# Performance work log

Measured on AMD Instinct MI355X. Metric: run time of the kernel, lower is better.

The kernel has to match this reference:

```python
import jax, jax.numpy as jnp
import numpy as np

N, E, IN, H, D, C = 30000, 400000, 128, 4, 64, 40
EPS = 1e-5
SLOPE = 0.2  # DGL GATv2Conv leaky_relu negative_slope default


def setup_inputs() -> dict:
    key = jax.random.key(0)
    ks = jax.random.split(key, 20)
    def rn(k, shape, s=0.05):
        return jax.random.normal(k, shape, jnp.float32) * s
    return {
        "x": jax.random.normal(ks[0], (N, IN), jnp.float32),
        "src": jax.random.randint(ks[1], (E,), 0, N),
        "dst": jax.random.randint(ks[2], (E,), 0, N),
        # layer 0: in=128 -> heads*64 (residual projection since 128 != 256)
        "W_src0": rn(ks[3], (IN, H * D)), "W_dst0": rn(ks[4], (IN, H * D)),
        "b0": jnp.zeros((H * D,), jnp.float32), "attn0": rn(ks[5], (H, D)),
        "res_W0": rn(ks[6], (IN, H * D)),
        # layer 1: 256 -> heads*64 (identity residual since 256 == 256)
        "W_src1": rn(ks[7], (H * D, H * D)), "W_dst1": rn(ks[8], (H * D, H * D)),
        "b1": jnp.zeros((H * D,), jnp.float32), "attn1": rn(ks[9], (H, D)),
        # layer 2: 256 -> heads*40 (residual projection)
        "W_src2": rn(ks[10], (H * D, H * C)), "W_dst2": rn(ks[11], (H * D, H * C)),
        "b2": jnp.zeros((H * C,), jnp.float32), "attn2": rn(ks[12], (H, C)),
        "res_W2": rn(ks[13], (H * D, H * C)),
        # batchnorm affine params (training-mode batch stats)
        "g0": jnp.ones((H * D,), jnp.float32), "be0": jnp.zeros((H * D,), jnp.float32),
        "g1": jnp.ones((H * D,), jnp.float32), "be1": jnp.zeros((H * D,), jnp.float32),
    }


def gatv2_layer(h, src, dst, Wsrc, Wdst, b, attn, resW, out_dim, relu_act):
    # DGL GATv2Conv: score_e = attn . leaky_relu(fc_src(h)[u] + fc_dst(h)[v])
    n = h.shape[0]
    fs = (h @ Wsrc).reshape(n, H, out_dim)
    fd = (h @ Wdst).reshape(n, H, out_dim)
    e = jax.nn.leaky_relu(fs[src] + fd[dst], SLOPE)      # [E, H, out]
    score = jnp.einsum("ehd,hd->eh", e, attn)            # [E, H]
    # segment softmax over incoming edges of each dst node
    m = jax.ops.segment_max(score, dst, num_segments=n)
    m = jnp.where(jnp.isfinite(m), m, 0.0)               # zero in-degree safety
    ex = jnp.exp(score - m[dst])
    denom = jax.ops.segment_sum(ex, dst, num_segments=n)
    alpha = ex / jnp.maximum(denom, 1e-9)[dst]
    rst = jax.ops.segment_sum(alpha[:, :, None] * fs[src], dst, num_segments=n)
    res = (h @ resW).reshape(n, H, out_dim) if resW is not None else h.reshape(n, H, out_dim)
    rst = rst + res + b.reshape(1, H, out_dim)
    return jax.nn.relu(rst) if relu_act else rst


def batchnorm(h, g, be):
    mu = h.mean(0)
    var = h.var(0)  # biased variance, as torch BN uses for normalization
    return g * (h - mu) * jax.lax.rsqrt(var + EPS) + be


def reference(x, src, dst, W_src0, W_dst0, b0, attn0, res_W0, W_src1, W_dst1, b1, attn1, W_src2, W_dst2, b2, attn2, res_W2, g0, be0, g1, be1):
    h = gatv2_layer(x, src, dst, W_src0, W_dst0, b0, attn0, res_W0, D, True)
    h = jax.nn.relu(batchnorm(h.reshape(N, H * D), g0, be0))  # dropout = identity (eval)
    h = gatv2_layer(h, src, dst, W_src1, W_dst1, b1, attn1, None, D, True)
    h = jax.nn.relu(batchnorm(h.reshape(N, H * D), g1, be1))
    h = gatv2_layer(h, src, dst, W_src2, W_dst2, b2, attn2, res_W2, C, False)
    h = h.mean(1)  # mean over heads -> [N, C]
    return jax.nn.log_softmax(h, axis=-1)
```

## Files before the change

kernel.cpp:

```cpp
#include <hip/hip_runtime.h>
#include <hip/hip_bf16.h>
#include <math.h>

#define NN 30000
#define EE 400000
#define INP 128
#define HH 4
#define DD 64
#define CC 40
#define HD 256
#define HC 160
#define NBLK 118

typedef unsigned short ushort;
typedef __attribute__((ext_vector_type(8))) short s8v;
typedef __attribute__((ext_vector_type(4))) float f4v;
typedef __attribute__((ext_vector_type(2))) float f2;


__device__ inline ushort bf16_of_float(float f) {
    __hip_bfloat16 b = __float2bfloat16(f);
    return *(ushort*)&b;
}
__device__ __forceinline__ float b2f(ushort u) { return __uint_as_float(((unsigned)u) << 16); }

__device__ __forceinline__ f2 cvt2v(unsigned d) {
    f2 r;
    r.x = __uint_as_float(d << 16);
    r.y = __uint_as_float(d & 0xFFFF0000u);
    return r;
}
__device__ __forceinline__ f2 splat2(float s) { f2 r = {s, s}; return r; }

__device__ __forceinline__ f2 pk_add(f2 a, f2 b) {
    f2 d; asm("v_pk_add_f32 %0, %1, %2" : "=v"(d) : "v"(a), "v"(b)); return d;
}
__device__ __forceinline__ f2 pk_mul(f2 a, f2 b) {
    f2 d; asm("v_pk_mul_f32 %0, %1, %2" : "=v"(d) : "v"(a), "v"(b)); return d;
}
__device__ __forceinline__ f2 pk_fma(f2 a, f2 b, f2 c) {
    f2 d; asm("v_pk_fma_f32 %0, %1, %2, %3" : "=v"(d) : "v"(a), "v"(b), "v"(c)); return d;
}
__device__ __forceinline__ f2 f2maxv(f2 a, f2 b) {
#if __has_builtin(__builtin_elementwise_max)
    return __builtin_elementwise_max(a, b);
#else
    f2 r; r.x = fmaxf(a.x, b.x); r.y = fmaxf(a.y, b.y); return r;
#endif
}

__device__ __forceinline__ void gld16(const void* g, void* l) {
    __builtin_amdgcn_global_load_lds((const __attribute__((address_space(1))) void*)g,
                                     (__attribute__((address_space(3))) void*)l, 16, 0, 0);
}

__device__ __forceinline__ float rowsum16(float x) {
    int t;
    t = __builtin_amdgcn_update_dpp(0, __float_as_int(x), 0x128, 0xF, 0xF, false); x += __int_as_float(t);
    t = __builtin_amdgcn_update_dpp(0, __float_as_int(x), 0x124, 0xF, 0xF, false); x += __int_as_float(t);
    t = __builtin_amdgcn_update_dpp(0, __float_as_int(x), 0x122, 0xF, 0xF, false); x += __int_as_float(t);
    t = __builtin_amdgcn_update_dpp(0, __float_as_int(x), 0x121, 0xF, 0xF, false); x += __int_as_float(t);
    return x;
}
__device__ __forceinline__ float rowmax16(float x) {
    int t;
    t = __builtin_amdgcn_update_dpp(0, __float_as_int(x), 0x128, 0xF, 0xF, false); x = fmaxf(x, __int_as_float(t));
    t = __builtin_amdgcn_update_dpp(0, __float_as_int(x), 0x124, 0xF, 0xF, false); x = fmaxf(x, __int_as_float(t));
    t = __builtin_amdgcn_update_dpp(0, __float_as_int(x), 0x122, 0xF, 0xF, false); x = fmaxf(x, __int_as_float(t));
    t = __builtin_amdgcn_update_dpp(0, __float_as_int(x), 0x121, 0xF, 0xF, false); x = fmaxf(x, __int_as_float(t));
    return x;
}

#define XB 3750
#define TB 1408
#define ZB 240

__global__ __launch_bounds__(256) void k_prep(const float* __restrict__ x, ushort* __restrict__ xc,
        const float* W0, const float* W1, const float* W2, const float* W3,
        const float* W4, const float* W5, const float* W6, const float* W7,
        ushort* bt0, ushort* bt1, ushort* bt2,
        int* __restrict__ zero_region,
        const float* b0, const float* a0, const float* b1, const float* a1,
        const float* b2, const float* a2, const float* g0, const float* be0,
        const float* g1, const float* be1, ushort* __restrict__ smallv) {
    int b = blockIdx.x, t = threadIdx.x;
    if (b < XB) {
        int i = b * 256 + t;
        if (i < NN * INP / 4) {
            float4 v = ((const float4*)x)[i];
            ushort4 o;
            o.x = bf16_of_float(v.x); o.y = bf16_of_float(v.y);
            o.z = bf16_of_float(v.z); o.w = bf16_of_float(v.w);
            ((ushort4*)xc)[i] = o;
        }
    } else if (b < XB + TB) {
        const float* Ws[8] = {W0, W1, W2, W3, W4, W5, W6, W7};
        int g = (b - XB) * 256 + t;
        if (g < 98304) {
            int seg = g >> 15, local = g & 32767;
            int n = local >> 7, k = local & 127;
            bt0[g] = bf16_of_float(Ws[seg][k * 256 + n]);
        } else if (g < 229376) {
            int gg = g - 98304;
            int seg = gg >> 16, local = gg & 65535;
            int n = local >> 8, k = local & 255;
            bt1[gg] = bf16_of_float(Ws[3 + seg][k * 256 + n]);
        } else if (g < 360448) {
            int gg = g - 229376;
            int n = gg >> 8, k = gg & 255;
            ushort val = 0;
            if (n < 480) {
                int seg = n / 160;
                int nn = n - seg * 160;
                val = bf16_of_float(Ws[5 + seg][k * 160 + nn]);
            }
            bt2[gg] = val;
        }
    } else if (b < XB + TB + ZB) {
        int i = (b - XB - TB) * 256 + t;
        if (i < 1024 + 2 * NN + 192) zero_region[i] = 0;
    } else {
        const float* ptrs[10] = {b0, a0, b1, a1, b2, a2, g0, be0, g1, be1};
        const int sz[10] = {256, 256, 256, 256, 160, 160, 256, 256, 256, 256};
        int off = 0;
        for (int j = 0; j < 10; j++) {
            if (t < sz[j]) smallv[off + t] = bf16_of_float(ptrs[j][t]);
            off += sz[j];
        }
    }
}


__global__ __launch_bounds__(256) void k_hist(const int* __restrict__ dst, int* __restrict__ cnt) {
    int e = blockIdx.x * 256 + threadIdx.x;
    if (e < EE) atomicAdd(&cnt[dst[e]], 1);
}

__global__ __launch_bounds__(256) void k_binbeg(const int* __restrict__ cnt, int* __restrict__ binCnt,
                                                int* __restrict__ beg, int* __restrict__ total) {
    __shared__ int lb[64];
    __shared__ int ss[256];
    __shared__ int base;
    int t = threadIdx.x;
    if (t < 64) lb[t] = 0;
    __syncthreads();
    int i = blockIdx.x * 256 + t;
    int c = (i < NN) ? cnt[i] : 0;
    int rc = (c + 3) & ~3;
    if (i < NN) atomicAdd(&lb[63 - min(c, 63)], 1);
    ss[t] = rc;
    __syncthreads();
    if (t < 64 && lb[t] > 0) atomicAdd(&binCnt[t], lb[t]);
    for (int o = 1; o < 256; o <<= 1) {
        int v = (t >= o) ? ss[t - o] : 0;
        __syncthreads();
        ss[t] += v;
        __syncthreads();
    }
    if (t == 255) base = atomicAdd(total, ss[255]);
    __syncthreads();
    if (i < NN) beg[i] = base + ss[t] - rc;
}

__global__ __launch_bounds__(256) void k_orderscatter(const int* __restrict__ cnt, const int* __restrict__ binCnt,
                                                      int* __restrict__ binPos, int* __restrict__ order,
                                                      const int* __restrict__ src, const int* __restrict__ dst,
                                                      const int* __restrict__ beg, int* __restrict__ pos,
                                                      int* __restrict__ srcs) {
    int t = threadIdx.x;
    if (blockIdx.x < NBLK) {
        __shared__ int lb[64], lbase[64], bpre[64];
        if (t < 64) { lb[t] = 0; bpre[t] = binCnt[t]; }
        __syncthreads();
        int i = blockIdx.x * 256 + t;
        int bin = 0, rank = 0;
        if (i < NN) {
            bin = 63 - min(cnt[i], 63);
            rank = atomicAdd(&lb[bin], 1);
        }
        for (int o = 1; o < 64; o <<= 1) {
            int v = (t >= o && t < 64) ? bpre[t - o] : 0;
            __syncthreads();
            if (t < 64) bpre[t] += v;
            __syncthreads();
        }
        if (t < 64 && lb[t] > 0)
            lbase[t] = bpre[t] - binCnt[t] + atomicAdd(&binPos[t], lb[t]);
        __syncthreads();
        if (i < NN) order[lbase[bin] + rank] = i;
    } else {
        int e = (blockIdx.x - NBLK) * 256 + t;
        if (e < EE) {
            int d = dst[e];
            int p = atomicAdd(&pos[d], 1);
            srcs[beg[d] + p] = src[e];
        }
    }
}


template<int K, int SEGW, int NSEG>
__global__ __launch_bounds__(256) void k_gemm_tiled(const ushort* __restrict__ A,
                                                    const ushort* __restrict__ Bt,
                                                    ushort* __restrict__ o0, ushort* __restrict__ o1,
                                                    ushort* __restrict__ o2) {
    __shared__ ushort As[128 * 32];
    __shared__ ushort Bs[128 * 32];
    int t = threadIdx.x;
    int wave = t >> 6, lane = t & 63;
    int m = lane & 15, q = lane >> 4;

    int nwg = gridDim.x * gridDim.y;
    int NB = gridDim.y;
    int ld = blockIdx.x + gridDim.x * blockIdx.y;
    int xcd = ld & 7, pos = ld >> 3;
    int qq = nwg >> 3, rr = nwg & 7;
    int base = (xcd < rr) ? xcd * (qq + 1) : rr * (qq + 1) + (xcd - rr) * qq;
    int swz = base + pos;
    int row0 = (swz / NB) * 128, col0 = (swz % NB) * 128;

    int wr = (wave >> 1) << 6, wc = (wave & 1) << 6;
    f4v acc[4][4] = {};
    int c1 = t, c2 = t + 256;
    int ar1 = min(row0 + (c1 >> 2), NN - 1);
    int ar2 = min(row0 + (c2 >> 2), NN - 1);
    const ushort* a1 = A + (size_t)ar1 * K + (c1 & 3) * 8;
    const ushort* a2 = A + (size_t)ar2 * K + (c2 & 3) * 8;
    const ushort* b1 = Bt + (size_t)(col0 + (c1 >> 2)) * K + (c1 & 3) * 8;
    const ushort* b2 = Bt + (size_t)(col0 + (c2 >> 2)) * K + (c2 & 3) * 8;
    int wbase = wave << 10;
    char* AsB = (char*)As;
    char* BsB = (char*)Bs;

#pragma unroll
    for (int kt = 0; kt < K; kt += 32) {
        __syncthreads();
        gld16(a1 + kt, AsB + wbase);
        gld16(a2 + kt, AsB + 4096 + wbase);
        gld16(b1 + kt, BsB + wbase);
        gld16(b2 + kt, BsB + 4096 + wbase);
        __syncthreads();
        s8v af[4], bg[4];
#pragma unroll
        for (int i = 0; i < 4; i++) af[i] = *(const s8v*)&As[(wr + i * 16 + m) * 32 + q * 8];
#pragma unroll
        for (int c = 0; c < 4; c++) bg[c] = *(const s8v*)&Bs[(wc + c * 16 + m) * 32 + q * 8];
#pragma unroll
        for (int i = 0; i < 4; i++)
#pragma unroll
            for (int c = 0; c < 4; c++)
                acc[i][c] = __builtin_amdgcn_mfma_f32_16x16x32_bf16(bg[c], af[i], acc[i][c], 0, 0, 0);
    }

#pragma unroll
    for (int c = 0; c < 4; c++) {
        int gcb = col0 + wc + c * 16;
        if (gcb < SEGW * NSEG) {
            int seg = gcb / SEGW;
            int colb = gcb - seg * SEGW + q * 4;
            ushort* op = seg == 0 ? o0 : (seg == 1 ? o1 : o2);
#pragma unroll
            for (int i = 0; i < 4; i++) {
                int gr = row0 + wr + i * 16 + m;
                if (gr < NN) {
                    ushort4 s4;
                    s4.x = bf16_of_float(acc[i][c][0]);
                    s4.y = bf16_of_float(acc[i][c][1]);
                    s4.z = bf16_of_float(acc[i][c][2]);
                    s4.w = bf16_of_float(acc[i][c][3]);
                    *(ushort4*)&op[(size_t)gr * SEGW + colb] = s4;
                }
            }
        }
    }
}


template<int DH, bool FINAL>
__global__ __launch_bounds__(256) void k_aggregate(const ushort* __restrict__ fs, const ushort* __restrict__ fd,
                                                   const ushort* __restrict__ res,
                                                   const ushort* __restrict__ attn,
                                                   const ushort* __restrict__ bias,
                                                   const int* __restrict__ beg, const int* __restrict__ cnt,
                                                   const int* __restrict__ srcs,
                                                   const int* __restrict__ order,
                                                   ushort* __restrict__ outb, float* __restrict__ outf) {
    constexpr int F = HH * DH;
    constexpr int JMAX = DH >> 2;
    int tt = threadIdx.x;
    int v = __builtin_amdgcn_readfirstlane(order[blockIdx.x * 4 + (tt >> 6)]);
    int lane = tt & 63;
    int h = lane >> 4, j = lane & 15;
    bool act = j < JMAX;
    unsigned off = h * DH + 4 * j;
    unsigned vbase = (unsigned)v * F + off;
    f2 fda = {0.f, 0.f}, fdb = {0.f, 0.f}, ava = {0.f, 0.f}, avb = {0.f, 0.f};
    if (act) {
        uint2 d = *(const uint2*)&fd[vbase];
        fda = cvt2v(d.x); fdb = cvt2v(d.y);
        uint2 a = *(const uint2*)&attn[off];
        const float LOG2E = 1.4426950408889634f;
        ava = cvt2v(a.x) * LOG2E; avb = cvt2v(a.y) * LOG2E;
    }
    const f2 c02 = {0.2f, 0.2f};
    float l = 0.f;
    f2 acca = {0.f, 0.f}, accb = {0.f, 0.f};
    int b0i = beg[v], end = b0i + cnt[v];

    auto dotlr = [&](const f2& ra, const f2& rb) -> float {
        f2 t0 = pk_add(ra, fda);
        f2 t1 = pk_add(rb, fdb);
        t0 = f2maxv(t0, pk_mul(t0, c02));
        t1 = f2maxv(t1, pk_mul(t1, c02));
        f2 p = pk_mul(ava, t0);
        p = pk_fma(avb, t1, p);
        return p.x + p.y;
    };
    auto edge4 = [&](const uint2& d0, const uint2& d1, const uint2& d2, const uint2& d3) {
        f2 a0 = cvt2v(d0.x), b0 = cvt2v(d0.y);
        f2 a1 = cvt2v(d1.x), b1 = cvt2v(d1.y);
        f2 a2 = cvt2v(d2.x), b2 = cvt2v(d2.y);
        f2 a3 = cvt2v(d3.x), b3 = cvt2v(d3.y);
        float p0 = rowsum16(dotlr(a0, b0));
        float p1 = rowsum16(dotlr(a1, b1));
        float p2 = rowsum16(dotlr(a2, b2));
        float p3 = rowsum16(dotlr(a3, b3));
        float w0 = __builtin_amdgcn_exp2f(p0), w1 = __builtin_amdgcn_exp2f(p1);
        float w2 = __builtin_amdgcn_exp2f(p2), w3 = __builtin_amdgcn_exp2f(p3);
        l += (w0 + w1) + (w2 + w3);
        f2 s0 = splat2(w0), s1 = splat2(w1), s2 = splat2(w2), s3 = splat2(w3);
        acca = pk_fma(s0, a0, acca); accb = pk_fma(s0, b0, accb);
        acca = pk_fma(s1, a1, acca); accb = pk_fma(s1, b1, accb);
        acca = pk_fma(s2, a2, acca); accb = pk_fma(s2, b2, accb);
        acca = pk_fma(s3, a3, acca); accb = pk_fma(s3, b3, accb);
    };

    int i = b0i;
    for (; i + 7 < end; i += 8) {
        int4 ua = *(const int4*)&srcs[i];
        int4 ub = *(const int4*)&srcs[i + 4];
        uint2 d0 = {0,0}, d1 = {0,0}, d2 = {0,0}, d3 = {0,0};
        uint2 d4 = {0,0}, d5 = {0,0}, d6 = {0,0}, d7 = {0,0};
        if (act) {
            d0 = *(const uint2*)&fs[(unsigned)ua.x * F + off];
            d1 = *(const uint2*)&fs[(unsigned)ua.y * F + off];
            d2 = *(const uint2*)&fs[(unsigned)ua.z * F + off];
            d3 = *(const uint2*)&fs[(unsigned)ua.w * F + off];
            d4 = *(const uint2*)&fs[(unsigned)ub.x * F + off];
            d5 = *(const uint2*)&fs[(unsigned)ub.y * F + off];
            d6 = *(const uint2*)&fs[(unsigned)ub.z * F + off];
            d7 = *(const uint2*)&fs[(unsigned)ub.w * F + off];
        }
        edge4(d0, d1, d2, d3);
        edge4(d4, d5, d6, d7);
    }
    for (; i + 3 < end; i += 4) {
        int4 ua = *(const int4*)&srcs[i];
        uint2 d0 = {0,0}, d1 = {0,0}, d2 = {0,0}, d3 = {0,0};
        if (act) {
            d0 = *(const uint2*)&fs[(unsigned)ua.x * F + off];
            d1 = *(const uint2*)&fs[(unsigned)ua.y * F + off];
            d2 = *(const uint2*)&fs[(unsigned)ua.z * F + off];
            d3 = *(const uint2*)&fs[(unsigned)ua.w * F + off];
        }
        edge4(d0, d1, d2, d3);
    }
    for (; i < end; i++) {
        f2 ra = splat2(0.f), rb = splat2(0.f);
        if (act) {
            uint2 d = *(const uint2*)&fs[(unsigned)srcs[i] * F + off];
            ra = cvt2v(d.x); rb = cvt2v(d.y);
        }
        float p0 = rowsum16(dotlr(ra, rb));
        float w0 = __builtin_amdgcn_exp2f(p0);
        l += w0;
        f2 s0 = splat2(w0);
        acca = pk_fma(s0, ra, acca);
        accb = pk_fma(s0, rb, accb);
    }

    float4 o4 = {0.f, 0.f, 0.f, 0.f};
    if (act) {
        float inv = 1.f / fmaxf(l, 1e-9f);
        uint2 rr = *(const uint2*)&res[vbase];
        f2 rl = cvt2v(rr.x), rh = cvt2v(rr.y);
        uint2 bb = *(const uint2*)&bias[off];
        f2 bl = cvt2v(bb.x), bh = cvt2v(bb.y);
        o4.x = acca.x * inv + rl.x + bl.x;
        o4.y = acca.y * inv + rl.y + bl.y;
        o4.z = accb.x * inv + rh.x + bh.x;
        o4.w = accb.y * inv + rh.y + bh.y;
        if (!FINAL) {
            o4.x = fmaxf(o4.x, 0.f); o4.y = fmaxf(o4.y, 0.f);
            o4.z = fmaxf(o4.z, 0.f); o4.w = fmaxf(o4.w, 0.f);
        }
    }
    if (!FINAL) {
        if (act) {
            ushort4 s4;
            s4.x = bf16_of_float(o4.x); s4.y = bf16_of_float(o4.y);
            s4.z = bf16_of_float(o4.z); s4.w = bf16_of_float(o4.w);
            *(ushort4*)&outb[vbase] = s4;
        }
    } else {
#pragma unroll
        for (int msk = 16; msk <= 32; msk <<= 1) {
            o4.x += __shfl_xor(o4.x, msk, 64);
            o4.y += __shfl_xor(o4.y, msk, 64);
            o4.z += __shfl_xor(o4.z, msk, 64);
            o4.w += __shfl_xor(o4.w, msk, 64);
        }
        float4 zv = make_float4(0.25f * o4.x, 0.25f * o4.y, 0.25f * o4.z, 0.25f * o4.w);
        float mx4 = act ? fmaxf(fmaxf(zv.x, zv.y), fmaxf(zv.z, zv.w)) : -1e30f;
        float mx = rowmax16(mx4);
        float es = 0.f;
        if (act) es = __expf(zv.x - mx) + __expf(zv.y - mx) + __expf(zv.z - mx) + __expf(zv.w - mx);
        float ssum = rowsum16(es);
        float lse = mx + logf(ssum);
        if (act && h == 0) {
            float4 w4 = make_float4(zv.x - lse, zv.y - lse, zv.z - lse, zv.w - lse);
            *(float4*)&outf[(size_t)v * CC + 4 * j] = w4;
        }
    }
}


__global__ __launch_bounds__(256) void k_bn_partial(const ushort* __restrict__ h, float* __restrict__ sum,
                                                    float* __restrict__ sumsq) {
    int c = threadIdx.x;
    int r0 = blockIdx.x * 128;
    int r1 = min(NN, r0 + 128);
    float s0 = 0.f, ss0 = 0.f, s1 = 0.f, ss1 = 0.f;
    int r = r0;
#pragma unroll 4
    for (; r + 1 < r1; r += 2) {
        float v0 = b2f(h[(size_t)r * HD + c]);
        float v1 = b2f(h[(size_t)(r + 1) * HD + c]);
        s0 += v0; ss0 = __fmaf_rn(v0, v0, ss0);
        s1 += v1; ss1 = __fmaf_rn(v1, v1, ss1);
    }
    if (r < r1) {
        float v0 = b2f(h[(size_t)r * HD + c]);
        s0 += v0; ss0 = __fmaf_rn(v0, v0, ss0);
    }
    atomicAdd(&sum[c], s0 + s1);
    atomicAdd(&sumsq[c], ss0 + ss1);
}


__global__ __launch_bounds__(256) void k_bn_norm(const ushort* __restrict__ hin, const float* __restrict__ sum,
                                                 const float* __restrict__ sumsq,
                                                 const ushort* __restrict__ g,
                                                 const ushort* __restrict__ be,
                                                 ushort* __restrict__ hbf) {
    int i4 = blockIdx.x * 256 + threadIdx.x;
    if (i4 < NN * HD / 4) {
        int base = i4 * 4;
        int c = base & (HD - 1);
        ushort4 hv = ((const ushort4*)hin)[i4];
        ushort4 ov;
        float vv[4] = {b2f(hv.x), b2f(hv.y), b2f(hv.z), b2f(hv.w)};
        ushort* po = (ushort*)&ov;
#pragma unroll
        for (int k = 0; k < 4; k++) {
            float mean = sum[c + k] * (1.0f / NN);
            float var = fmaxf(sumsq[c + k] * (1.0f / NN) - mean * mean, 0.f);
            float y = b2f(g[c + k]) * (vv[k] - mean) * rsqrtf(var + 1e-5f) + b2f(be[c + k]);
            po[k] = bf16_of_float(fmaxf(y, 0.f));
        }
        ((ushort4*)hbf)[i4] = ov;
    }
}


static inline char* alignup(char* p) { return (char*)(((size_t)p + 255) & ~(size_t)255); }

extern "C" void kernel_launch(void* const* d_in, const int* in_sizes, int n_in,
                              void* d_out, int out_size, void* d_ws, size_t ws_size,
                              hipStream_t stream) {
    const float* x     = (const float*)d_in[0];
    const int*  src    = (const int*)d_in[1];
    const int*  dst    = (const int*)d_in[2];
    const float* Wsrc0 = (const float*)d_in[3];
    const float* Wdst0 = (const float*)d_in[4];
    const float* b0    = (const float*)d_in[5];
    const float* attn0 = (const float*)d_in[6];
    const float* resW0 = (const float*)d_in[7];
    const float* Wsrc1 = (const float*)d_in[8];
    const float* Wdst1 = (const float*)d_in[9];
    const float* b1    = (const float*)d_in[10];
    const float* attn1 = (const float*)d_in[11];
    const float* Wsrc2 = (const float*)d_in[12];
    const float* Wdst2 = (const float*)d_in[13];
    const float* b2    = (const float*)d_in[14];
    const float* attn2 = (const float*)d_in[15];
    const float* resW2 = (const float*)d_in[16];
    const float* g0    = (const float*)d_in[17];
    const float* be0   = (const float*)d_in[18];
    const float* g1    = (const float*)d_in[19];
    const float* be1   = (const float*)d_in[20];

    char* w = (char*)d_ws;
    const size_t NF = (size_t)NN * HD;
    ushort* fsb = (ushort*)w; w += NF * 2;
    ushort* fdb = (ushort*)w; w += NF * 2;
    ushort* resb= (ushort*)w; w += NF * 2;
    ushort* hag = (ushort*)w; w += NF * 2;
    ushort* hbf = (ushort*)w; w += NF * 2;
    ushort* xc  = (ushort*)w; w += (size_t)NN * INP * 2;
    ushort* bt0 = (ushort*)w; w += 768 * 128 * 2;
    ushort* bt1 = (ushort*)w; w += 512 * 256 * 2;
    ushort* bt2 = (ushort*)w; w += 512 * 256 * 2;
    ushort* smallv = (ushort*)w; w += 2368 * 2; w = alignup(w);
    float* bnstats = (float*)w; w += 1024 * 4;
    int* cnt    = (int*)w; w += NN * 4;
    int* pos    = (int*)w; w += NN * 4;
    int* binCnt = (int*)w; w += 64 * 4;
    int* binPos = (int*)w; w += 64 * 4;
    int* total  = (int*)w; w += 64 * 4; w = alignup(w);
    int* beg    = (int*)w; w += NN * 4; w = alignup(w);
    int* order  = (int*)w; w += NN * 4; w = alignup(w);
    int* srcs   = (int*)w; w += (size_t)(EE + 3 * NN + 64) * 4;

    const ushort* c_b0    = smallv + 0;
    const ushort* c_attn0 = smallv + 256;
    const ushort* c_b1    = smallv + 512;
    const ushort* c_attn1 = smallv + 768;
    const ushort* c_b2    = smallv + 1024;
    const ushort* c_attn2 = smallv + 1184;
    const ushort* c_g0    = smallv + 1344;
    const ushort* c_be0   = smallv + 1600;
    const ushort* c_g1    = smallv + 1856;
    const ushort* c_be1   = smallv + 2112;

    k_prep<<<XB + TB + ZB + 1, 256, 0, stream>>>(x, xc,
        Wsrc0, Wdst0, resW0, Wsrc1, Wdst1, Wsrc2, Wdst2, resW2, bt0, bt1, bt2,
        (int*)bnstats,
        b0, attn0, b1, attn1, b2, attn2, g0, be0, g1, be1, smallv);

    k_hist<<<(EE + 255) / 256, 256, 0, stream>>>(dst, cnt);
    k_binbeg<<<NBLK, 256, 0, stream>>>(cnt, binCnt, beg, total);
    k_orderscatter<<<NBLK + (EE + 255) / 256, 256, 0, stream>>>(cnt, binCnt, binPos, order,
                                                                src, dst, beg, pos, srcs);

    const int MB = (NN + 127) / 128;

    k_gemm_tiled<128, 256, 3><<<dim3(MB, 6), 256, 0, stream>>>(xc, bt0, fsb, fdb, resb);
    k_aggregate<DD, false><<<NN / 4, 256, 0, stream>>>(fsb, fdb, resb, c_attn0, c_b0,
        beg, cnt, srcs, order, hag, nullptr);
    k_bn_partial<<<MB, 256, 0, stream>>>(hag, bnstats, bnstats + 256);
    k_bn_norm<<<(int)((NF / 4 + 255) / 256), 256, 0, stream>>>(hag, bnstats, bnstats + 256,
                                                               c_g0, c_be0, hbf);

    k_gemm_tiled<256, 256, 2><<<dim3(MB, 4), 256, 0, stream>>>(hbf, bt1, fsb, fdb, nullptr);
    k_aggregate<DD, false><<<NN / 4, 256, 0, stream>>>(fsb, fdb, hbf, c_attn1, c_b1,
        beg, cnt, srcs, order, hag, nullptr);
    k_bn_partial<<<MB, 256, 0, stream>>>(hag, bnstats + 512, bnstats + 768);
    k_bn_norm<<<(int)((NF / 4 + 255) / 256), 256, 0, stream>>>(hag, bnstats + 512, bnstats + 768,
                                                               c_g1, c_be1, hbf);

    k_gemm_tiled<256, 160, 3><<<dim3(MB, 4), 256, 0, stream>>>(hbf, bt2, fsb, fdb, resb);
    k_aggregate<CC, true><<<NN / 4, 256, 0, stream>>>(fsb, fdb, resb, c_attn2, c_b2,
        beg, cnt, srcs, order, nullptr, (float*)d_out);
}
```

Baseline: 358.3 us.

## Add specialized 64-dim GATv2 aggregation kernel processing four edges per wave

Adds a dedicated aggregation kernel for the two 64-wide layers. Each wave splits into four 16-lane groups, each handling a different incoming edge, with 16 features per lane. Scores are reduced with DPP quad sums and exponentiated with exp2, using attention weights prescaled by log2(e). There is no running max subtraction (an unstabilized softmax), and partial accumulators are combined across groups with xor shuffles at the end. This aims to raise memory-level parallelism on the edge gathers and cut the online-softmax bookkeeping. The risk is overflow if scores get large, plus wasted lanes on low-degree tail iterations.

```diff
diff --git a/kernel.cpp b/kernel.cpp
--- a/kernel.cpp
+++ b/kernel.cpp
@@ -68,6 +68,12 @@
     t = __builtin_amdgcn_update_dpp(0, __float_as_int(x), 0x124, 0xF, 0xF, false); x = fmaxf(x, __int_as_float(t));
     t = __builtin_amdgcn_update_dpp(0, __float_as_int(x), 0x122, 0xF, 0xF, false); x = fmaxf(x, __int_as_float(t));
     t = __builtin_amdgcn_update_dpp(0, __float_as_int(x), 0x121, 0xF, 0xF, false); x = fmaxf(x, __int_as_float(t));
+    return x;
+}
+__device__ __forceinline__ float qsum4(float x) {
+    int t;
+    t = __builtin_amdgcn_update_dpp(0, __float_as_int(x), 0xB1, 0xF, 0xF, false); x += __int_as_float(t);
+    t = __builtin_amdgcn_update_dpp(0, __float_as_int(x), 0x4E, 0xF, 0xF, false); x += __int_as_float(t);
     return x;
 }
 
@@ -272,6 +278,104 @@
                 }
             }
         }
+    }
+}
+
+
+__global__ __launch_bounds__(256) void k_aggregate64(
+        const ushort* __restrict__ fs, const ushort* __restrict__ fd,
+        const ushort* __restrict__ res, const ushort* __restrict__ attn,
+        const ushort* __restrict__ bias,
+        const int* __restrict__ beg, const int* __restrict__ cnt,
+        const int* __restrict__ srcs, const int* __restrict__ order,
+        ushort* __restrict__ outb) {
+    int tt = threadIdx.x;
+    int v = __builtin_amdgcn_readfirstlane(order[blockIdx.x * 4 + (tt >> 6)]);
+    int lane = tt & 63;
+    int g = lane >> 4, s = lane & 15;
+    unsigned soff = (unsigned)s * 16;
+    unsigned vb = (unsigned)v * HD;
+    const float LOG2E = 1.4426950408889634f;
+    const f2 c02 = {0.2f, 0.2f};
+
+    uint4 fdA = *(const uint4*)&fd[vb + soff];
+    uint4 fdB = *(const uint4*)&fd[vb + soff + 8];
+    uint4 avA = *(const uint4*)&attn[soff];
+    uint4 avB = *(const uint4*)&attn[soff + 8];
+    f2 fd0 = cvt2v(fdA.x), fd1 = cvt2v(fdA.y), fd2 = cvt2v(fdA.z), fd3 = cvt2v(fdA.w);
+    f2 fd4 = cvt2v(fdB.x), fd5 = cvt2v(fdB.y), fd6 = cvt2v(fdB.z), fd7 = cvt2v(fdB.w);
+    f2 av0 = cvt2v(avA.x) * LOG2E, av1 = cvt2v(avA.y) * LOG2E;
+    f2 av2 = cvt2v(avA.z) * LOG2E, av3 = cvt2v(avA.w) * LOG2E;
+    f2 av4 = cvt2v(avB.x) * LOG2E, av5 = cvt2v(avB.y) * LOG2E;
+    f2 av6 = cvt2v(avB.z) * LOG2E, av7 = cvt2v(avB.w) * LOG2E;
+
+    f2 acc0 = {0.f,0.f}, acc1 = {0.f,0.f}, acc2 = {0.f,0.f}, acc3 = {0.f,0.f};
+    f2 acc4 = {0.f,0.f}, acc5 = {0.f,0.f}, acc6 = {0.f,0.f}, acc7 = {0.f,0.f};
+    float l = 0.f;
+    int b0i = beg[v], end = b0i + cnt[v];
+
+    for (int i = b0i; i < end; i += 4) {
+        int rem = end - i;
+        int ge = (g < rem) ? g : (rem - 1);
+        unsigned u = (unsigned)srcs[i + ge];
+        const ushort* rp = fs + (size_t)u * HD + soff;
+        uint4 RA = *(const uint4*)rp;
+        uint4 RB = *(const uint4*)(rp + 8);
+        f2 r0 = cvt2v(RA.x), r1 = cvt2v(RA.y), r2 = cvt2v(RA.z), r3 = cvt2v(RA.w);
+        f2 r4 = cvt2v(RB.x), r5 = cvt2v(RB.y), r6 = cvt2v(RB.z), r7 = cvt2v(RB.w);
+        f2 t, p;
+        t = pk_add(r0, fd0); t = f2maxv(t, pk_mul(t, c02)); p = pk_mul(av0, t);
+        t = pk_add(r1, fd1); t = f2maxv(t, pk_mul(t, c02)); p = pk_fma(av1, t, p);
+        t = pk_add(r2, fd2); t = f2maxv(t, pk_mul(t, c02)); p = pk_fma(av2, t, p);
+        t = pk_add(r3, fd3); t = f2maxv(t, pk_mul(t, c02)); p = pk_fma(av3, t, p);
+        t = pk_add(r4, fd4); t = f2maxv(t, pk_mul(t, c02)); p = pk_fma(av4, t, p);
+        t = pk_add(r5, fd5); t = f2maxv(t, pk_mul(t, c02)); p = pk_fma(av5, t, p);
+        t = pk_add(r6, fd6); t = f2maxv(t, pk_mul(t, c02)); p = pk_fma(av6, t, p);
+        t = pk_add(r7, fd7); t = f2maxv(t, pk_mul(t, c02)); p = pk_fma(av7, t, p);
+        float sc = p.x + p.y;
+        sc = qsum4(sc);
+        sc = (g < rem) ? sc : -1e30f;
+        float w = __builtin_amdgcn_exp2f(sc);
+        l += w;
+        f2 sw = splat2(w);
+        acc0 = pk_fma(sw, r0, acc0); acc1 = pk_fma(sw, r1, acc1);
+        acc2 = pk_fma(sw, r2, acc2); acc3 = pk_fma(sw, r3, acc3);
+        acc4 = pk_fma(sw, r4, acc4); acc5 = pk_fma(sw, r5, acc5);
+        acc6 = pk_fma(sw, r6, acc6); acc7 = pk_fma(sw, r7, acc7);
+    }
+
+#pragma unroll
+    for (int msk = 16; msk <= 32; msk <<= 1) {
+        l += __shfl_xor(l, msk, 64);
+        acc0.x += __shfl_xor(acc0.x, msk, 64); acc0.y += __shfl_xor(acc0.y, msk, 64);
+        acc1.x += __shfl_xor(acc1.x, msk, 64); acc1.y += __shfl_xor(acc1.y, msk, 64);
+        acc2.x += __shfl_xor(acc2.x, msk, 64); acc2.y += __shfl_xor(acc2.y, msk, 64);
+        acc3.x += __shfl_xor(acc3.x, msk, 64); acc3.y += __shfl_xor(acc3.y, msk, 64);
+        acc4.x += __shfl_xor(acc4.x, msk, 64); acc4.y += __shfl_xor(acc4.y, msk, 64);
+        acc5.x += __shfl_xor(acc5.x, msk, 64); acc5.y += __shfl_xor(acc5.y, msk, 64);
+        acc6.x += __shfl_xor(acc6.x, msk, 64); acc6.y += __shfl_xor(acc6.y, msk, 64);
+        acc7.x += __shfl_xor(acc7.x, msk, 64); acc7.y += __shfl_xor(acc7.y, msk, 64);
+    }
+    float inv = 1.f / fmaxf(l, 1e-9f);
+
+    uint4 rrA = *(const uint4*)&res[vb + soff];
+    uint4 rrB = *(const uint4*)&res[vb + soff + 8];
+    uint4 bbA = *(const uint4*)&bias[soff];
+    uint4 bbB = *(const uint4*)&bias[soff + 8];
+    auto outw = [&](f2 a, unsigned rd, unsigned bd) -> unsigned {
+        f2 rs = cvt2v(rd), bb = cvt2v(bd);
+        float ox = fmaxf(a.x * inv + rs.x + bb.x, 0.f);
+        float oy = fmaxf(a.y * inv + rs.y + bb.y, 0.f);
+        return (unsigned)bf16_of_float(ox) | ((unsigned)bf16_of_float(oy) << 16);
+    };
+    uint4 oA, oB;
+    oA.x = outw(acc0, rrA.x, bbA.x); oA.y = outw(acc1, rrA.y, bbA.y);
+    oA.z = outw(acc2, rrA.z, bbA.z); oA.w = outw(acc3, rrA.w, bbA.w);
+    oB.x = outw(acc4, rrB.x, bbB.x); oB.y = outw(acc5, rrB.y, bbB.y);
+    oB.z = outw(acc6, rrB.z, bbB.z); oB.w = outw(acc7, rrB.w, bbB.w);
+    if (g == 0) {
+        *(uint4*)&outb[vb + soff] = oA;
+        *(uint4*)&outb[vb + soff + 8] = oB;
     }
 }
 
@@ -546,15 +650,15 @@
     const int MB = (NN + 127) / 128;
 
     k_gemm_tiled<128, 256, 3><<<dim3(MB, 6), 256, 0, stream>>>(xc, bt0, fsb, fdb, resb);
-    k_aggregate<DD, false><<<NN / 4, 256, 0, stream>>>(fsb, fdb, resb, c_attn0, c_b0,
-        beg, cnt, srcs, order, hag, nullptr);
+    k_aggregate64<<<NN / 4, 256, 0, stream>>>(fsb, fdb, resb, c_attn0, c_b0,
+        beg, cnt, srcs, order, hag);
     k_bn_partial<<<MB, 256, 0, stream>>>(hag, bnstats, bnstats + 256);
     k_bn_norm<<<(int)((NF / 4 + 255) / 256), 256, 0, stream>>>(hag, bnstats, bnstats + 256,
                                                                c_g0, c_be0, hbf);
 
     k_gemm_tiled<256, 256, 2><<<dim3(MB, 4), 256, 0, stream>>>(hbf, bt1, fsb, fdb, nullptr);
-    k_aggregate<DD, false><<<NN / 4, 256, 0, stream>>>(fsb, fdb, hbf, c_attn1, c_b1,
-        beg, cnt, srcs, order, hag, nullptr);
+    k_aggregate64<<<NN / 4, 256, 0, stream>>>(fsb, fdb, hbf, c_attn1, c_b1,
+        beg, cnt, srcs, order, hag);
     k_bn_partial<<<MB, 256, 0, stream>>>(hag, bnstats + 512, bnstats + 768);
     k_bn_norm<<<(int)((NF / 4 + 255) / 256), 256, 0, stream>>>(hag, bnstats + 512, bnstats + 768,
                                                                c_g1, c_be1, hbf);
```

Result: no change. 364.2 us (+1.6%).
